# Optimization experiments

Hardware: AMD Instinct MI355X
Metric: run time of the kernel (lower is better)

## Reference

```python
import jax, jax.numpy as jnp
import numpy as np

N, E, G = 50000, 1600000, 512
IN, H = 16, 128


def setup_inputs() -> dict:
    key = jax.random.key(0)
    ks = jax.random.split(key, 10)
    x = jax.random.normal(ks[0], (N, IN), dtype=jnp.float32)
    edge_index = jax.random.randint(ks[1], (2, E), 0, N, dtype=jnp.int64)
    batch = jnp.sort(jax.random.randint(ks[2], (N,), 0, G, dtype=jnp.int64))
    s = lambda k, sh, fan: jax.random.normal(k, sh, dtype=jnp.float32) / np.sqrt(fan)
    return {
        "x": x, "edge_index": edge_index, "batch": batch,
        "W1": s(ks[3], (IN, H), IN), "b1": jnp.zeros((H,), jnp.float32),
        "W2": s(ks[4], (H, H), H), "b2": jnp.zeros((H,), jnp.float32),
        "Wlab": s(ks[5], (H, 1), H), "blab": jnp.zeros((1,), jnp.float32),
        "Wd1": s(ks[6], (H, 64), H), "bd1": jnp.zeros((64,), jnp.float32),
        "Wd2": s(ks[7], (64, 2), 64), "bd2": jnp.zeros((2,), jnp.float32),
    }


def _gcn_conv(x, src, dst, norm, W, b, num_nodes):
    # x' = sum_{(s,d) in E+selfloops} norm_e * (x W)[s] scattered to d, + b
    h = x @ W                                  # [N, H]
    msgs = h[src] * norm[:, None]              # [E+N, H]
    out = jax.ops.segment_sum(msgs, dst, num_segments=num_nodes)
    return out + b


def _forward(x, edge_index, batch, W1, b1, W2, b2, Wlab, blab, Wd1, bd1, Wd2, bd2):
    num_nodes = x.shape[0]
    loop = jnp.arange(num_nodes, dtype=edge_index.dtype)
    src = jnp.concatenate([edge_index[0], loop])
    dst = jnp.concatenate([edge_index[1], loop])
    # symmetric GCN normalization: deg computed at dst after self-loops
    deg = jax.ops.segment_sum(jnp.ones_like(dst, dtype=x.dtype), dst,
                              num_segments=num_nodes)
    dinv = jnp.where(deg > 0, jax.lax.rsqrt(deg), 0.0)
    norm = dinv[src] * dinv[dst]               # [E+N]

    h = jax.nn.relu(_gcn_conv(x, src, dst, norm, W1, b1, num_nodes))
    h = jax.nn.relu(_gcn_conv(h, src, dst, norm, W2, b2, num_nodes))

    # global mean pool over graphs
    sums = jax.ops.segment_sum(h, batch, num_segments=G)        # [G, H]
    cnts = jax.ops.segment_sum(jnp.ones((num_nodes,), h.dtype), batch,
                               num_segments=G)
    pooled = sums / jnp.maximum(cnts, 1.0)[:, None]

    label_out = jax.nn.sigmoid(pooled @ Wlab + blab)            # [G, 1]
    # grad_reverse is identity in the forward pass
    dom_out = jax.nn.relu(pooled @ Wd1 + bd1) @ Wd2 + bd2       # [G, 2]
    return label_out, dom_out


def reference(x, edge_index, batch, W1, b1, W2, b2, Wlab, blab, Wd1, bd1, Wd2, bd2):
    return _forward(x, edge_index, batch, W1, b1, W2, b2, Wlab, blab,
                    Wd1, bd1, Wd2, bd2)
```

## Files before the change

### kernel.cpp

```cpp
#include <hip/hip_runtime.h>
#include <math.h>


#define BCAP 12288

typedef __attribute__((ext_vector_type(8))) short short8;
typedef __attribute__((ext_vector_type(4))) float f32x4;

__device__ __forceinline__ void bf4acc(uint2 u, float* a) {
    a[0] += __uint_as_float(u.x << 16);
    a[1] += __uint_as_float(u.x & 0xffff0000u);
    a[2] += __uint_as_float(u.y << 16);
    a[3] += __uint_as_float(u.y & 0xffff0000u);
}

__device__ __forceinline__ unsigned short bf1(float a) {
    unsigned ua = __float_as_uint(a);
    return (unsigned short)((ua + 0x7fffu + ((ua >> 16) & 1u)) >> 16);
}

__global__ __launch_bounds__(256) void k_bfill(
        const int* __restrict__ ei, int* __restrict__ bcnt,
        unsigned* __restrict__ col1,
        const int* __restrict__ batch, int* __restrict__ gptr,
        float* __restrict__ gsum, const float* __restrict__ W2,
        unsigned short* __restrict__ W2bf,
        int E, int chunk, int NB, int N, int G) {
    __shared__ int bins[256];
    __shared__ int base[256];
    for (int t = threadIdx.x; t < NB; t += 256) bins[t] = 0;
    __syncthreads();
    const int e0 = blockIdx.x * chunk;
    int e1 = e0 + chunk; if (e1 > E) e1 = E;
    for (int j = e0 + (int)threadIdx.x; j < e1; j += 256)
        atomicAdd(&bins[ei[E + j] >> 8], 1);
    __syncthreads();
    for (int t = threadIdx.x; t < NB; t += 256) {
        base[t] = bins[t] ? atomicAdd(&bcnt[t], bins[t]) : 0;
        bins[t] = 0;
    }
    __syncthreads();
    for (int j = e0 + (int)threadIdx.x; j < e1; j += 256) {
        int d = ei[E + j];
        int s = ei[j];
        int b = d >> 8;
        int pos = base[b] + atomicAdd(&bins[b], 1);
        if (pos < BCAP)
            col1[(size_t)b * BCAP + pos] = ((unsigned)(d & 255) << 16) | (unsigned)s;
    }

    const int gid = blockIdx.x * 256 + threadIdx.x;
    const int gsz = gridDim.x * 256;
    for (int i = gid; i < G * 32; i += gsz)
        ((float4*)gsum)[i] = make_float4(0.f, 0.f, 0.f, 0.f);
    for (int i = gid; i < 16384; i += gsz) {
        const int f2 = i >> 7, f1 = i & 127;
        W2bf[i] = bf1(W2[f1 * 128 + f2]);
    }
    for (int g = gid; g <= G; g += gsz) {
        int lo = 0, hi = N;
        while (lo < hi) {
            int mid = (lo + hi) >> 1;
            if (batch[mid] < g) lo = mid + 1; else hi = mid;
        }
        gptr[g] = lo;
    }
}

__global__ __launch_bounds__(256) void k_bsort(const unsigned* __restrict__ col1,
                                               const int* __restrict__ bcnt,
                                               int* __restrict__ col,
                                               int* __restrict__ rowptr,
                                               float* __restrict__ dinv,
                                               const float* __restrict__ x,
                                               unsigned short* __restrict__ xsb,
                                               int N, int E, int NB) {
    __shared__ unsigned ec[BCAP];
    __shared__ int bins[256], sc[256];
    __shared__ float dvb[256];
    const int b = blockIdx.x, t = threadIdx.x;

    {
        int v = (t < NB) ? bcnt[t] : 0;
        bins[t] = v;
        __syncthreads();
        for (int off = 1; off < 256; off <<= 1) {
            int add = (t >= off) ? bins[t - off] : 0;
            __syncthreads();
            bins[t] += add;
            __syncthreads();
        }
    }
    const int s0 = (b == 0) ? 0 : bins[b - 1];
    int cnt = bcnt[b];
    if (cnt > BCAP) cnt = BCAP;
    __syncthreads();

    for (int i = t; i < cnt; i += 256) ec[i] = col1[(size_t)b * BCAP + i];
    bins[t] = 0;
    __syncthreads();
    for (int i = t; i < cnt; i += 256) atomicAdd(&bins[ec[i] >> 16], 1);
    __syncthreads();
    const int v = bins[t];
    sc[t] = v;
    __syncthreads();
    for (int off = 1; off < 256; off <<= 1) {
        int add = (t >= off) ? sc[t - off] : 0;
        __syncthreads();
        sc[t] += add;
        __syncthreads();
    }
    const int ex = sc[t] - v;
    __syncthreads();
    sc[t] = ex;
    bins[t] = 0;
    const float dv = rsqrtf((float)(v + 1));
    dvb[t] = dv;
    const int n0 = b * 256;
    if (n0 + t < N) {
        rowptr[n0 + t] = s0 + ex;
        dinv[n0 + t] = dv;
    }
    if (b == 0 && t == 0) rowptr[N] = E;
    __syncthreads();
    for (int i = t; i < cnt; i += 256) {
        unsigned e = ec[i];
        int dl = e >> 16;
        int p = sc[dl] + atomicAdd(&bins[dl], 1);
        col[s0 + p] = (int)(e & 0xffffu);
    }
    int nn = N - n0; if (nn > 256) nn = 256;
    const int lim = nn * 16;
    for (int i = t; i < lim; i += 256) {
        float vx = x[(size_t)n0 * 16 + i] * dvb[i >> 4];
        xsb[(size_t)n0 * 16 + i] = bf1(vx);
    }
}

__global__ __launch_bounds__(512, 4) void k_l12g(
        const int* __restrict__ rowptr, const int* __restrict__ col,
        const unsigned short* __restrict__ xsb,
        const float* __restrict__ dinv,
        const float* __restrict__ W1, const float* __restrict__ b1,
        const unsigned short* __restrict__ W2bf,
        unsigned short* __restrict__ ht1b, int N) {
    __shared__ __align__(16) unsigned short W2s[128 * 136];
    __shared__ __align__(16) unsigned short h1b[64 * 136];
    __shared__ __align__(16) float arow[64 * 16];
    __shared__ float dv[64];
    const int tid = threadIdx.x;
    const int n0 = blockIdx.x * 64;
    const int w = tid >> 6, lane = tid & 63;

    for (int i = tid; i < 2048; i += 512) {
        const int f2 = i >> 4, seg = i & 15;
        *(uint4*)&W2s[f2 * 136 + seg * 8] = ((const uint4*)W2bf)[i];
    }
    if (tid < 64) dv[tid] = (n0 + tid < N) ? dinv[n0 + tid] : 0.f;

    {
        const int nd = lane >> 3, sub = lane & 7;
        const int slot = sub >> 2, qq = sub & 3;
        const int j = w * 8 + nd;
        const int n = n0 + j;
        float a[4] = {0.f, 0.f, 0.f, 0.f};
        if (n < N) {
            const int r1 = rowptr[n + 1];
            for (int e = rowptr[n] + slot; e < r1; e += 2)
                bf4acc(*(const uint2*)(xsb + (size_t)col[e] * 16 + qq * 4), a);
        }
#pragma unroll
        for (int i = 0; i < 4; ++i) a[i] += __shfl_xor(a[i], 4);
        if (slot == 0) {
            if (n < N) {
                bf4acc(*(const uint2*)(xsb + (size_t)n * 16 + qq * 4), a);
                *(float4*)&arow[j * 16 + qq * 4] = make_float4(a[0], a[1], a[2], a[3]);
            } else {
                *(float4*)&arow[j * 16 + qq * 4] = make_float4(0.f, 0.f, 0.f, 0.f);
            }
        }
    }
    const int f = tid & 127, jg = tid >> 7;
    float w1r[16];
#pragma unroll
    for (int k = 0; k < 16; ++k) w1r[k] = W1[k * 128 + f];
    const float bias = b1[f];
    __syncthreads();

#pragma unroll 4
    for (int j = jg * 16; j < jg * 16 + 16; ++j) {
        float s = 0.f;
#pragma unroll
        for (int k = 0; k < 16; ++k) s += arow[j * 16 + k] * w1r[k];
        h1b[j * 136 + f] = bf1(fmaxf(dv[j] * s + bias, 0.f));
    }
    __syncthreads();

    const int mt = w & 3, nh = w >> 2;
    const int lm = lane & 15, quad = lane >> 4;
    f32x4 acc[4];
#pragma unroll
    for (int t = 0; t < 4; ++t) acc[t] = (f32x4){0.f, 0.f, 0.f, 0.f};
#pragma unroll
    for (int kb = 0; kb < 4; ++kb) {
        const short8 af = *(const short8*)&h1b[(mt * 16 + lm) * 136 + kb * 32 + quad * 8];
#pragma unroll
        for (int t = 0; t < 4; ++t) {
            const short8 bfv = *(const short8*)&W2s[(nh * 64 + t * 16 + lm) * 136 + kb * 32 + quad * 8];
            acc[t] = __builtin_amdgcn_mfma_f32_16x16x32_bf16(af, bfv, acc[t], 0, 0, 0);
        }
    }
#pragma unroll
    for (int t = 0; t < 4; ++t) {
        const int f2 = nh * 64 + t * 16 + lm;
#pragma unroll
        for (int r = 0; r < 4; ++r) {
            const int j = mt * 16 + quad * 4 + r;
            const int n = n0 + j;
            if (n < N)
                ht1b[(size_t)n * 128 + f2] = bf1(acc[t][r] * dv[j]);
        }
    }
}

__global__ __launch_bounds__(512) void k_gat128pool(
        const int* __restrict__ rowptr, const int* __restrict__ col,
        const unsigned short* __restrict__ ht1b,
        const float* __restrict__ dinv, const float* __restrict__ b2,
        const int* __restrict__ batch, float* __restrict__ gsum, int N) {
    __shared__ __align__(16) float h2s[8][128];
    __shared__ int bats[8];
    const int wave = threadIdx.x >> 6, lane = threadIdx.x & 63;
    const int half = lane >> 5, q = lane & 31;
    const int n = blockIdx.x * 8 + wave;
    float a[4] = {0.f, 0.f, 0.f, 0.f};
    if (n < N) {
        const int r0 = rowptr[n], r1 = rowptr[n + 1];
        int j = r0 + half;
        while (j + 6 < r1) {
            int s0 = col[j], s1 = col[j + 2], s2 = col[j + 4], s3 = col[j + 6];
            uint2 u0 = *(const uint2*)(ht1b + (size_t)s0 * 128 + q * 4);
            uint2 u1 = *(const uint2*)(ht1b + (size_t)s1 * 128 + q * 4);
            uint2 u2 = *(const uint2*)(ht1b + (size_t)s2 * 128 + q * 4);
            uint2 u3 = *(const uint2*)(ht1b + (size_t)s3 * 128 + q * 4);
            bf4acc(u0, a); bf4acc(u1, a); bf4acc(u2, a); bf4acc(u3, a);
            j += 8;
        }
        while (j < r1) {
            bf4acc(*(const uint2*)(ht1b + (size_t)col[j] * 128 + q * 4), a);
            j += 2;
        }
        if (half == 0)
            bf4acc(*(const uint2*)(ht1b + (size_t)n * 128 + q * 4), a);
    }
#pragma unroll
    for (int i = 0; i < 4; ++i) a[i] += __shfl_xor(a[i], 32);
    if (half == 0) {
        if (n < N) {
            const float d = dinv[n];
            const float4 bb = *(const float4*)(b2 + q * 4);
            h2s[wave][q * 4 + 0] = fmaxf(a[0] * d + bb.x, 0.f);
            h2s[wave][q * 4 + 1] = fmaxf(a[1] * d + bb.y, 0.f);
            h2s[wave][q * 4 + 2] = fmaxf(a[2] * d + bb.z, 0.f);
            h2s[wave][q * 4 + 3] = fmaxf(a[3] * d + bb.w, 0.f);
            if (q == 0) bats[wave] = batch[n];
        } else {
            h2s[wave][q * 4 + 0] = 0.f; h2s[wave][q * 4 + 1] = 0.f;
            h2s[wave][q * 4 + 2] = 0.f; h2s[wave][q * 4 + 3] = 0.f;
            if (q == 0) bats[wave] = -1;
        }
    }
    __syncthreads();
    if (threadIdx.x < 32) {
        const int qq = threadIdx.x;
        int bprev = bats[0];
        float4 acc4 = *(const float4*)&h2s[0][qq * 4];
#pragma unroll
        for (int wv = 1; wv < 8; ++wv) {
            const int bw = bats[wv];
            const float4 rv = *(const float4*)&h2s[wv][qq * 4];
            if (bw == bprev) {
                acc4.x += rv.x; acc4.y += rv.y; acc4.z += rv.z; acc4.w += rv.w;
            } else {
                if (bprev >= 0) {
                    float* gs = gsum + (size_t)bprev * 128 + qq * 4;
                    unsafeAtomicAdd(gs + 0, acc4.x); unsafeAtomicAdd(gs + 1, acc4.y);
                    unsafeAtomicAdd(gs + 2, acc4.z); unsafeAtomicAdd(gs + 3, acc4.w);
                }
                bprev = bw; acc4 = rv;
            }
        }
        if (bprev >= 0) {
            float* gs = gsum + (size_t)bprev * 128 + qq * 4;
            unsafeAtomicAdd(gs + 0, acc4.x); unsafeAtomicAdd(gs + 1, acc4.y);
            unsafeAtomicAdd(gs + 2, acc4.z); unsafeAtomicAdd(gs + 3, acc4.w);
        }
    }
}

__global__ __launch_bounds__(128) void k_head(
        const float* __restrict__ gsum, const int* __restrict__ gptr,
        const float* __restrict__ Wlab, const float* __restrict__ blab,
        const float* __restrict__ Wd1, const float* __restrict__ bd1,
        const float* __restrict__ Wd2, const float* __restrict__ bd2,
        float* __restrict__ out, int G) {
    __shared__ float sp[128];
    __shared__ float red[128];
    __shared__ float hd[64];
    const int g = blockIdx.x, t = threadIdx.x;
    const float cnt = (float)(gptr[g + 1] - gptr[g]);
    const float invc = 1.f / fmaxf(cnt, 1.f);
    const float pooled = gsum[g * 128 + t] * invc;
    sp[t] = pooled;
    red[t] = pooled * Wlab[t];
    __syncthreads();
    for (int off = 64; off > 0; off >>= 1) {
        if (t < off) red[t] += red[t + off];
        __syncthreads();
    }
    if (t == 0) {
        float z = red[0] + blab[0];
        out[g] = 1.f / (1.f + expf(-z));
    }
    if (t < 64) {
        float s = bd1[t];
        for (int f = 0; f < 128; ++f) s += sp[f] * Wd1[f * 64 + t];
        hd[t] = fmaxf(s, 0.f);
    }
    __syncthreads();
    if (t < 2) {
        float s = bd2[t];
        for (int j = 0; j < 64; ++j) s += hd[j] * Wd2[j * 2 + t];
        out[G + g * 2 + t] = s;
    }
}

extern "C" void kernel_launch(void* const* d_in, const int* in_sizes, int n_in,
                              void* d_out, int out_size, void* d_ws, size_t ws_size,
                              hipStream_t stream) {
    const float* x     = (const float*)d_in[0];
    const int*   ei    = (const int*)d_in[1];
    const int*   batch = (const int*)d_in[2];
    const float* W1    = (const float*)d_in[3];
    const float* b1    = (const float*)d_in[4];
    const float* W2    = (const float*)d_in[5];
    const float* b2    = (const float*)d_in[6];
    const float* Wlab  = (const float*)d_in[7];
    const float* blab  = (const float*)d_in[8];
    const float* Wd1   = (const float*)d_in[9];
    const float* bd1   = (const float*)d_in[10];
    const float* Wd2   = (const float*)d_in[11];
    const float* bd2   = (const float*)d_in[12];
    float* out = (float*)d_out;

    const int N = in_sizes[0] / 16;
    const int E = in_sizes[1] / 2;
    const int G = out_size / 3;
    const int NB = (N + 255) >> 8;

    char* p = (char*)d_ws;
    auto carve = [&](size_t bytes) {
        void* r = (void*)p;
        p += (bytes + 255) & ~(size_t)255;
        return r;
    };
    int*      bcnt   = (int*)     carve(256 * 4);
    unsigned* col1   = (unsigned*)carve((size_t)NB * BCAP * 4);
    int*      col    = (int*)     carve((size_t)E * 4);
    int*      rowptr = (int*)     carve((size_t)(N + 1) * 4);
    int*      gptr   = (int*)     carve((size_t)(G + 1) * 4);
    float*    dinv   = (float*)   carve((size_t)N * 4);
    unsigned short* xsb  = (unsigned short*)carve((size_t)N * 16 * 2);
    unsigned short* W2bf = (unsigned short*)carve(128 * 128 * 2);
    unsigned short* ht1b = (unsigned short*)carve((size_t)N * 128 * 2);
    float*    gsum   = (float*)   carve((size_t)G * 128 * 4);

    const int FB = 256;
    const int chunk = (E + FB - 1) / FB;

    hipMemsetAsync(bcnt, 0, 256 * 4, stream);
    k_bfill  <<<FB, 256, 0, stream>>>(ei, bcnt, col1, batch, gptr, gsum, W2,
                                      W2bf, E, chunk, NB, N, G);
    k_bsort  <<<NB, 256, 0, stream>>>(col1, bcnt, col, rowptr, dinv, x, xsb,
                                      N, E, NB);
    k_l12g   <<<(N + 63) / 64, 512, 0, stream>>>(rowptr, col, xsb, dinv,
                                                 W1, b1, W2bf, ht1b, N);
    k_gat128pool<<<(N + 7) / 8, 512, 0, stream>>>(rowptr, col, ht1b, dinv, b2,
                                                  batch, gsum, N);
    k_head   <<<G, 128, 0, stream>>>(gsum, gptr, Wlab, blab, Wd1, bd1, Wd2,
                                     bd2, out, G);
}
```

Measured before the change: 230.1 us.

## Halve bucket size in CSR build, widen layer-1 gathers, split pooling launch

The destination bucket width drops from 256 to 128 nodes, which doubles the bucket count to 391 and halves BCAP. The counting sort runs with 512 threads per block, and its scan now covers up to 512 buckets. The layer-1 gather now loads 16-byte uint4 rows with 4 edge slots instead of 8-byte loads with 2 slots, so it needs an extra shuffle reduction. The layer-2 gather/pool kernel is split into two launches over halves of the nodes, which adds launch overhead for no clear benefit and may be a probe. Smaller buckets give the sort more blocks and less shared memory per block, but BCAP=6144 leaves less headroom: about 4096 edges are expected per bucket.

```diff
diff --git a/kernel.cpp b/kernel.cpp
--- a/kernel.cpp
+++ b/kernel.cpp
@@ -2,7 +2,7 @@
 #include <math.h>
 
 
-#define BCAP 12288
+#define BCAP 6144
 
 typedef __attribute__((ext_vector_type(8))) short short8;
 typedef __attribute__((ext_vector_type(4))) float f32x4;
@@ -12,6 +12,17 @@
     a[1] += __uint_as_float(u.x & 0xffff0000u);
     a[2] += __uint_as_float(u.y << 16);
     a[3] += __uint_as_float(u.y & 0xffff0000u);
+}
+
+__device__ __forceinline__ void bf8acc(uint4 u, float* a) {
+    a[0] += __uint_as_float(u.x << 16);
+    a[1] += __uint_as_float(u.x & 0xffff0000u);
+    a[2] += __uint_as_float(u.y << 16);
+    a[3] += __uint_as_float(u.y & 0xffff0000u);
+    a[4] += __uint_as_float(u.z << 16);
+    a[5] += __uint_as_float(u.z & 0xffff0000u);
+    a[6] += __uint_as_float(u.w << 16);
+    a[7] += __uint_as_float(u.w & 0xffff0000u);
 }
 
 __device__ __forceinline__ unsigned short bf1(float a) {
@@ -26,14 +37,14 @@
         float* __restrict__ gsum, const float* __restrict__ W2,
         unsigned short* __restrict__ W2bf,
         int E, int chunk, int NB, int N, int G) {
-    __shared__ int bins[256];
-    __shared__ int base[256];
+    __shared__ int bins[512];
+    __shared__ int base[512];
     for (int t = threadIdx.x; t < NB; t += 256) bins[t] = 0;
     __syncthreads();
     const int e0 = blockIdx.x * chunk;
     int e1 = e0 + chunk; if (e1 > E) e1 = E;
     for (int j = e0 + (int)threadIdx.x; j < e1; j += 256)
-        atomicAdd(&bins[ei[E + j] >> 8], 1);
+        atomicAdd(&bins[ei[E + j] >> 7], 1);
     __syncthreads();
     for (int t = threadIdx.x; t < NB; t += 256) {
         base[t] = bins[t] ? atomicAdd(&bcnt[t], bins[t]) : 0;
@@ -43,10 +54,10 @@
     for (int j = e0 + (int)threadIdx.x; j < e1; j += 256) {
         int d = ei[E + j];
         int s = ei[j];
-        int b = d >> 8;
+        int b = d >> 7;
         int pos = base[b] + atomicAdd(&bins[b], 1);
         if (pos < BCAP)
-            col1[(size_t)b * BCAP + pos] = ((unsigned)(d & 255) << 16) | (unsigned)s;
+            col1[(size_t)b * BCAP + pos] = ((unsigned)(d & 127) << 16) | (unsigned)s;
     }
 
     const int gid = blockIdx.x * 256 + threadIdx.x;
@@ -67,7 +78,7 @@
     }
 }
 
-__global__ __launch_bounds__(256) void k_bsort(const unsigned* __restrict__ col1,
+__global__ __launch_bounds__(512) void k_bsort(const unsigned* __restrict__ col1,
                                                const int* __restrict__ bcnt,
                                                int* __restrict__ col,
                                                int* __restrict__ rowptr,
@@ -76,62 +87,62 @@
                                                unsigned short* __restrict__ xsb,
                                                int N, int E, int NB) {
     __shared__ unsigned ec[BCAP];
-    __shared__ int bins[256], sc[256];
-    __shared__ float dvb[256];
+    __shared__ int bins[512];
+    __shared__ int sc[128], cur[128];
+    __shared__ float dvb[128];
     const int b = blockIdx.x, t = threadIdx.x;
 
-    {
-        int v = (t < NB) ? bcnt[t] : 0;
-        bins[t] = v;
+    bins[t] = (t < NB) ? bcnt[t] : 0;
+    __syncthreads();
+    for (int off = 1; off < 512; off <<= 1) {
+        int add = (t >= off) ? bins[t - off] : 0;
         __syncthreads();
-        for (int off = 1; off < 256; off <<= 1) {
-            int add = (t >= off) ? bins[t - off] : 0;
-            __syncthreads();
-            bins[t] += add;
-            __syncthreads();
-        }
+        bins[t] += add;
+        __syncthreads();
     }
     const int s0 = (b == 0) ? 0 : bins[b - 1];
     int cnt = bcnt[b];
     if (cnt > BCAP) cnt = BCAP;
-    __syncthreads();
-
-    for (int i = t; i < cnt; i += 256) ec[i] = col1[(size_t)b * BCAP + i];
-    bins[t] = 0;
-    __syncthreads();
-    for (int i = t; i < cnt; i += 256) atomicAdd(&bins[ec[i] >> 16], 1);
-    __syncthreads();
-    const int v = bins[t];
-    sc[t] = v;
-    __syncthreads();
-    for (int off = 1; off < 256; off <<= 1) {
-        int add = (t >= off) ? sc[t - off] : 0;
+    if (t < 128) cur[t] = 0;
+    __syncthreads();
+
+    for (int i = t; i < cnt; i += 512) ec[i] = col1[(size_t)b * BCAP + i];
+    __syncthreads();
+    for (int i = t; i < cnt; i += 512) atomicAdd(&cur[ec[i] >> 16], 1);
+    __syncthreads();
+    const int v = (t < 128) ? cur[t] : 0;
+    if (t < 128) sc[t] = v;
+    __syncthreads();
+    for (int off = 1; off < 128; off <<= 1) {
+        int add = (t >= off && t < 128) ? sc[t - off] : 0;
         __syncthreads();
-        sc[t] += add;
+        if (t < 128) sc[t] += add;
         __syncthreads();
     }
-    const int ex = sc[t] - v;
-    __syncthreads();
-    sc[t] = ex;
-    bins[t] = 0;
-    const float dv = rsqrtf((float)(v + 1));
-    dvb[t] = dv;
-    const int n0 = b * 256;
-    if (n0 + t < N) {
-        rowptr[n0 + t] = s0 + ex;
-        dinv[n0 + t] = dv;
+    const int ex = (t < 128) ? (sc[t] - v) : 0;
+    __syncthreads();
+    const int n0 = b * 128;
+    if (t < 128) {
+        sc[t] = ex;
+        cur[t] = 0;
+        const float dv = rsqrtf((float)(v + 1));
+        dvb[t] = dv;
+        if (n0 + t < N) {
+            rowptr[n0 + t] = s0 + ex;
+            dinv[n0 + t] = dv;
+        }
     }
     if (b == 0 && t == 0) rowptr[N] = E;
     __syncthreads();
-    for (int i = t; i < cnt; i += 256) {
+    for (int i = t; i < cnt; i += 512) {
         unsigned e = ec[i];
         int dl = e >> 16;
-        int p = sc[dl] + atomicAdd(&bins[dl], 1);
+        int p = sc[dl] + atomicAdd(&cur[dl], 1);
         col[s0 + p] = (int)(e & 0xffffu);
     }
-    int nn = N - n0; if (nn > 256) nn = 256;
+    int nn = N - n0; if (nn > 128) nn = 128;
     const int lim = nn * 16;
-    for (int i = t; i < lim; i += 256) {
+    for (int i = t; i < lim; i += 512) {
         float vx = x[(size_t)n0 * 16 + i] * dvb[i >> 4];
         xsb[(size_t)n0 * 16 + i] = bf1(vx);
     }
@@ -160,23 +171,30 @@
 
     {
         const int nd = lane >> 3, sub = lane & 7;
-        const int slot = sub >> 2, qq = sub & 3;
+        const int slot = sub >> 1, qq = sub & 1;
         const int j = w * 8 + nd;
         const int n = n0 + j;
-        float a[4] = {0.f, 0.f, 0.f, 0.f};
+        float a[8] = {0.f, 0.f, 0.f, 0.f, 0.f, 0.f, 0.f, 0.f};
         if (n < N) {
             const int r1 = rowptr[n + 1];
-            for (int e = rowptr[n] + slot; e < r1; e += 2)
-                bf4acc(*(const uint2*)(xsb + (size_t)col[e] * 16 + qq * 4), a);
-        }
-#pragma unroll
-        for (int i = 0; i < 4; ++i) a[i] += __shfl_xor(a[i], 4);
+            for (int e = rowptr[n] + slot; e < r1; e += 4)
+                bf8acc(*(const uint4*)(xsb + (size_t)col[e] * 16 + qq * 8), a);
+        }
+#pragma unroll
+        for (int i = 0; i < 8; ++i) {
+            a[i] += __shfl_xor(a[i], 2);
+            a[i] += __shfl_xor(a[i], 4);
+        }
         if (slot == 0) {
             if (n < N) {
-                bf4acc(*(const uint2*)(xsb + (size_t)n * 16 + qq * 4), a);
-                *(float4*)&arow[j * 16 + qq * 4] = make_float4(a[0], a[1], a[2], a[3]);
+                bf8acc(*(const uint4*)(xsb + (size_t)n * 16 + qq * 8), a);
+                *(float4*)&arow[j * 16 + qq * 8] =
+                    make_float4(a[0], a[1], a[2], a[3]);
+                *(float4*)&arow[j * 16 + qq * 8 + 4] =
+                    make_float4(a[4], a[5], a[6], a[7]);
             } else {
-                *(float4*)&arow[j * 16 + qq * 4] = make_float4(0.f, 0.f, 0.f, 0.f);
+                *(float4*)&arow[j * 16 + qq * 8] = make_float4(0.f, 0.f, 0.f, 0.f);
+                *(float4*)&arow[j * 16 + qq * 8 + 4] = make_float4(0.f, 0.f, 0.f, 0.f);
             }
         }
     }
@@ -227,12 +245,13 @@
         const int* __restrict__ rowptr, const int* __restrict__ col,
         const unsigned short* __restrict__ ht1b,
         const float* __restrict__ dinv, const float* __restrict__ b2,
-        const int* __restrict__ batch, float* __restrict__ gsum, int N) {
+        const int* __restrict__ batch, float* __restrict__ gsum,
+        int N, int nbase) {
     __shared__ __align__(16) float h2s[8][128];
     __shared__ int bats[8];
     const int wave = threadIdx.x >> 6, lane = threadIdx.x & 63;
     const int half = lane >> 5, q = lane & 31;
-    const int n = blockIdx.x * 8 + wave;
+    const int n = nbase + blockIdx.x * 8 + wave;
     float a[4] = {0.f, 0.f, 0.f, 0.f};
     if (n < N) {
         const int r0 = rowptr[n], r1 = rowptr[n + 1];
@@ -356,7 +375,7 @@
     const int N = in_sizes[0] / 16;
     const int E = in_sizes[1] / 2;
     const int G = out_size / 3;
-    const int NB = (N + 255) >> 8;
+    const int NB = (N + 127) >> 7;
 
     char* p = (char*)d_ws;
     auto carve = [&](size_t bytes) {
@@ -364,7 +383,7 @@
         p += (bytes + 255) & ~(size_t)255;
         return r;
     };
-    int*      bcnt   = (int*)     carve(256 * 4);
+    int*      bcnt   = (int*)     carve(512 * 4);
     unsigned* col1   = (unsigned*)carve((size_t)NB * BCAP * 4);
     int*      col    = (int*)     carve((size_t)E * 4);
     int*      rowptr = (int*)     carve((size_t)(N + 1) * 4);
@@ -378,15 +397,21 @@
     const int FB = 256;
     const int chunk = (E + FB - 1) / FB;
 
-    hipMemsetAsync(bcnt, 0, 256 * 4, stream);
+    const int NA = ((N / 2) + 7) & ~7;
+    const int blocksA = NA / 8;
+    const int blocksB = (N - NA + 7) / 8;
+
+    hipMemsetAsync(bcnt, 0, 512 * 4, stream);
     k_bfill  <<<FB, 256, 0, stream>>>(ei, bcnt, col1, batch, gptr, gsum, W2,
                                       W2bf, E, chunk, NB, N, G);
-    k_bsort  <<<NB, 256, 0, stream>>>(col1, bcnt, col, rowptr, dinv, x, xsb,
+    k_bsort  <<<NB, 512, 0, stream>>>(col1, bcnt, col, rowptr, dinv, x, xsb,
                                       N, E, NB);
     k_l12g   <<<(N + 63) / 64, 512, 0, stream>>>(rowptr, col, xsb, dinv,
                                                  W1, b1, W2bf, ht1b, N);
-    k_gat128pool<<<(N + 7) / 8, 512, 0, stream>>>(rowptr, col, ht1b, dinv, b2,
-                                                  batch, gsum, N);
+    k_gat128pool<<<blocksA, 512, 0, stream>>>(rowptr, col, ht1b, dinv, b2,
+                                              batch, gsum, N, 0);
+    k_gat128pool<<<blocksB, 512, 0, stream>>>(rowptr, col, ht1b, dinv, b2,
+                                              batch, gsum, N, NA);
     k_head   <<<G, 128, 0, stream>>>(gsum, gptr, Wlab, blab, Wd1, bd1, Wd2,
                                      bd2, out, G);
 }
```

After: 237.0 us. 3.0% more time.
